# Optimization experiments

Measured on AMD Instinct MI355X. Metric: run time of the kernel, lower is better.

Reference implementation:

```python
import jax, jax.numpy as jnp
import numpy as np

B, T, D = 2, 2048, 2048
H, KVH, HD = 32, 8, 64
N_REP = H // KVH


def setup_inputs() -> dict:
    key = jax.random.key(0)
    ks = jax.random.split(key, 7)
    x = jax.random.normal(ks[0], (B, T, D), dtype=jnp.float32)
    # rope tables: [max_seq, head_dim//2]
    cos = jax.random.uniform(ks[1], (T, HD // 2), dtype=jnp.float32, minval=-1.0, maxval=1.0)
    sin = jax.random.uniform(ks[2], (T, HD // 2), dtype=jnp.float32, minval=-1.0, maxval=1.0)
    s = 0.02
    wq = jax.random.normal(ks[3], (D, H * HD), dtype=jnp.float32) * s
    wk = jax.random.normal(ks[4], (D, KVH * HD), dtype=jnp.float32) * s
    wv = jax.random.normal(ks[5], (D, KVH * HD), dtype=jnp.float32) * s
    wo = jax.random.normal(ks[6], (H * HD, D), dtype=jnp.float32) * s
    return {"x": x, "cos": cos, "sin": sin, "wq": wq, "wk": wk, "wv": wv, "wo": wo}


def _rotate(t):
    h = t.shape[-1] // 2
    return jnp.concatenate([-t[..., h:], t[..., :h]], axis=-1)


def reference(x, cos, sin, wq, wk, wv, wo):
    b, t, _ = x.shape
    # projections -> [B, heads, T, HD]
    q = (x @ wq).reshape(b, t, H, HD).transpose(0, 2, 1, 3)
    k = (x @ wk).reshape(b, t, KVH, HD).transpose(0, 2, 1, 3)
    v = (x @ wv).reshape(b, t, KVH, HD).transpose(0, 2, 1, 3)
    # rope: cos/sin tiled (concat) to full head_dim, broadcast over batch/head
    cos_f = jnp.tile(cos[:t], (1, 2))[None, None]  # [1,1,T,HD]
    sin_f = jnp.tile(sin[:t], (1, 2))[None, None]
    q = q * cos_f + _rotate(q) * sin_f
    k = k * cos_f + _rotate(k) * sin_f
    # GQA: repeat kv heads
    k = jnp.repeat(k, N_REP, axis=1)
    v = jnp.repeat(v, N_REP, axis=1)
    scale = 1.0 / np.sqrt(HD).astype(np.float32)
    scores = jnp.einsum('bhqd,bhkd->bhqk', q, k) * scale
    causal = jnp.tril(jnp.ones((t, t), dtype=bool))
    scores = jnp.where(causal, scores, jnp.float32(-1e30))
    attn = jax.nn.softmax(scores, axis=-1)
    out = jnp.einsum('bhqk,bhkd->bhqd', attn, v)
    out = out.transpose(0, 2, 1, 3).reshape(b, t, H * HD)
    return out @ wo
```

## Files before the change

kernel.cpp:

```cpp
#include <hip/hip_runtime.h>
#include <hip/hip_bf16.h>
#include <cstdint>

typedef unsigned short u16;
typedef unsigned int u32;
typedef __bf16 bf16x8 __attribute__((ext_vector_type(8)));
typedef float f32x4 __attribute__((ext_vector_type(4)));
typedef float f32x16 __attribute__((ext_vector_type(16)));

#define BATCH 2
#define SEQ 2048
#define DMODEL 2048
#define NH 32
#define NKVH 8
#define HD 64
#define NQROWS (BATCH*SEQ)
#define QCOLS (NH*HD)
#define KVCOLS (NKVH*HD)
#define NCAT (QCOLS+2*KVCOLS)

static __device__ __forceinline__ u16 f2bf(float f) {
  u32 u = __float_as_uint(f);
  return (u16)((u + 0x7fffu + ((u >> 16) & 1u)) >> 16);
}

#define GLOAD16(gp, lp) __builtin_amdgcn_global_load_lds( \
    (const __attribute__((address_space(1))) void*)(gp),  \
    (__attribute__((address_space(3))) void*)(lp), 16, 0, 0)

__global__ __launch_bounds__(256) void k_cvt_bf16(const float* __restrict__ in,
                                                  u16* __restrict__ out, int n4) {
  int i = blockIdx.x * 256 + threadIdx.x;
  if (i >= n4) return;
  float4 v = reinterpret_cast<const float4*>(in)[i];
  ushort4 o;
  o.x = f2bf(v.x); o.y = f2bf(v.y); o.z = f2bf(v.z); o.w = f2bf(v.w);
  reinterpret_cast<ushort4*>(out)[i] = o;
}

__global__ __launch_bounds__(256) void k_transpose_w(const float* __restrict__ in,
                                                     u16* __restrict__ out, int R, int C) {
  __shared__ float tile[32][33];
  int c0 = blockIdx.x * 32, r0 = blockIdx.y * 32;
  int tx = threadIdx.x, ty = threadIdx.y;
#pragma unroll
  for (int i = 0; i < 4; i++)
    tile[ty * 4 + i][tx] = in[(size_t)(r0 + ty * 4 + i) * C + c0 + tx];
  __syncthreads();
#pragma unroll
  for (int i = 0; i < 4; i++)
    out[(size_t)(c0 + ty * 4 + i) * R + r0 + tx] = f2bf(tile[tx][ty * 4 + i]);
}

template<int EPI>
__global__ __launch_bounds__(256) void k_gemm(const u16* __restrict__ A,
                                              const u16* __restrict__ BT,
                                              void* __restrict__ Cout,
                                              int M, int N, int K,
                                              const float* __restrict__ cosb,
                                              const float* __restrict__ sinb,
                                              u16* __restrict__ dstK,
                                              u16* __restrict__ dstV) {
  __shared__ __align__(16) u16 As[2][128 * 32];
  __shared__ __align__(16) u16 Bs[2][128 * 32];
  const int tid = threadIdx.x;
  const int w = tid >> 6, l = tid & 63;
  const int l15 = l & 15, l4 = l >> 4;

  const int nwg = gridDim.x * gridDim.y;
  int hwid = blockIdx.y * gridDim.x + blockIdx.x;
  int wk = (hwid & 7) * (nwg >> 3) + (hwid >> 3);
  const int bx = wk % gridDim.x, by = wk / gridDim.x;

  const int m0 = by * 128, n0 = bx * 128;
  const int wr = w >> 1, wc = w & 1;

  const u16* ga = A + (size_t)(m0 + w * 32 + (l >> 2)) * K + (l & 3) * 8;
  const u16* gb = BT + (size_t)(n0 + w * 32 + (l >> 2)) * K + (l & 3) * 8;
  const int af_off = (wr * 64 + l15) * 32 + l4 * 8;
  const int bf_off = (wc * 64 + l15) * 32 + l4 * 8;

  auto stage = [&](int buf, int kt) {
    const u16* ga_ = ga + kt;
    const u16* gb_ = gb + kt;
    u16* asb = &As[buf][w * 1024];
    u16* bsb = &Bs[buf][w * 1024];
    GLOAD16(ga_, asb);
    GLOAD16(ga_ + 16 * (size_t)K, asb + 512);
    GLOAD16(gb_, bsb);
    GLOAD16(gb_ + 16 * (size_t)K, bsb + 512);
  };

  f32x4 acc[4][4] = {};
  stage(0, 0);
  __syncthreads();

  int cur = 0;
  for (int kt = 0; kt < K; kt += 32) {
    if (kt + 32 < K) stage(cur ^ 1, kt + 32);
    bf16x8 af[4], bfv[4];
#pragma unroll
    for (int mi = 0; mi < 4; mi++)
      af[mi] = *reinterpret_cast<const bf16x8*>(&As[cur][af_off + mi * 512]);
#pragma unroll
    for (int ni = 0; ni < 4; ni++)
      bfv[ni] = *reinterpret_cast<const bf16x8*>(&Bs[cur][bf_off + ni * 512]);
#pragma unroll
    for (int mi = 0; mi < 4; mi++)
#pragma unroll
      for (int ni = 0; ni < 4; ni++)
        acc[mi][ni] = __builtin_amdgcn_mfma_f32_16x16x32_bf16(af[mi], bfv[ni], acc[mi][ni], 0, 0, 0);
    __syncthreads();
    cur ^= 1;
  }

  const int row0 = m0 + wr * 64 + l4 * 4;
  const int col0 = n0 + wc * 64 + l15;
  if constexpr (EPI == 1) {
    float* C = (float*)Cout;
#pragma unroll
    for (int mi = 0; mi < 4; mi++)
#pragma unroll
      for (int ni = 0; ni < 4; ni++)
#pragma unroll
        for (int j = 0; j < 4; j++)
          C[(size_t)(row0 + mi * 16 + j) * N + col0 + ni * 16] = acc[mi][ni][j];
  } else {
    if (n0 < QCOLS + KVCOLS) {
#pragma unroll
      for (int mi = 0; mi < 4; mi++)
#pragma unroll
        for (int j = 0; j < 4; j++) {
          int t = (row0 + mi * 16 + j) & (SEQ - 1);
#pragma unroll
          for (int ni = 0; ni < 2; ni++) {
            int d = ni * 16 + l15;
            float c = cosb[t * 32 + d], s = sinb[t * 32 + d];
            float a = acc[mi][ni][j], bb = acc[mi][ni + 2][j];
            acc[mi][ni][j]     = a * c - bb * s;
            acc[mi][ni + 2][j] = bb * c + a * s;
          }
        }
      if (n0 < QCOLS) {
        const float QSC = 0.125f * 1.44269504088896f;
        u16* C = (u16*)Cout;
#pragma unroll
        for (int mi = 0; mi < 4; mi++)
#pragma unroll
          for (int ni = 0; ni < 4; ni++)
#pragma unroll
            for (int j = 0; j < 4; j++)
              C[(size_t)(row0 + mi * 16 + j) * QCOLS + col0 + ni * 16] = f2bf(acc[mi][ni][j] * QSC);
      } else {
        int kc0 = col0 - QCOLS;
#pragma unroll
        for (int mi = 0; mi < 4; mi++)
#pragma unroll
          for (int ni = 0; ni < 4; ni++)
#pragma unroll
            for (int j = 0; j < 4; j++)
              dstK[(size_t)(row0 + mi * 16 + j) * KVCOLS + kc0 + ni * 16] = f2bf(acc[mi][ni][j]);
      }
    } else {
      int vc0 = col0 - (QCOLS + KVCOLS);
#pragma unroll
      for (int mi = 0; mi < 4; mi++) {
        int row = row0 + mi * 16;
        int b = row >> 11, t = row & (SEQ - 1);
#pragma unroll
        for (int ni = 0; ni < 4; ni++) {
          ushort4 v;
          v.x = f2bf(acc[mi][ni][0]);
          v.y = f2bf(acc[mi][ni][1]);
          v.z = f2bf(acc[mi][ni][2]);
          v.w = f2bf(acc[mi][ni][3]);
          *reinterpret_cast<ushort4*>(&dstV[((size_t)b * KVCOLS + vc0 + ni * 16) * SEQ + t]) = v;
        }
      }
    }
  }
}

__global__ __launch_bounds__(128, 3) void k_attn(const u16* __restrict__ Q,
                                                 const u16* __restrict__ K,
                                                 const u16* __restrict__ VT,
                                                 u16* __restrict__ AO) {
  __shared__ __align__(16) u16 Ks[2][4096];
  __shared__ __align__(16) u16 Vs[2][4096];
  const int tid = threadIdx.x;
  const int w = tid >> 6, l = tid & 63;
  const int lo = l & 31, hi = l >> 5;
  const int bh = blockIdx.y;
  const int b = bh >> 5, h = bh & 31, g = h >> 2;
  const int srow = l >> 3;
  const int scol = l & 7;

  const u16* Kbase = K + ((size_t)b * SEQ) * KVCOLS + g * 64;
  const u16* Vbase = VT + ((size_t)(b * KVCOLS + g * 64)) * SEQ;

  for (int half = 0; half < 2; half++) {
    const int qt = half ? (31 - blockIdx.x) : blockIdx.x;
    const int qbase = qt * 64 + w * 32;
    const int nkc = qt + 1;
    const int qloc = w * 32 + lo;

    bf16x8 qf[4];
    {
      const u16* qp = Q + (size_t)(b * SEQ + qbase + lo) * QCOLS + h * 64 + hi * 8;
#pragma unroll
      for (int kb = 0; kb < 4; kb++)
        qf[kb] = *reinterpret_cast<const bf16x8*>(qp + kb * 16);
    }
    f32x16 oacc[2] = {};
    float ls0 = 0.f, ls1 = 0.f;

#pragma unroll
    for (int i = 0; i < 4; i++) {
      int r = w * 32 + i * 8 + srow;
      int cs = scol ^ (srow & 7);
      GLOAD16(Kbase + (size_t)r * KVCOLS + cs * 8, &Ks[0][(w * 32 + i * 8) * 64 + l * 8]);
      GLOAD16(Vbase + (size_t)r * SEQ + cs * 8, &Vs[0][(w * 32 + i * 8) * 64 + l * 8]);
    }
    __syncthreads();

    for (int kc = 0; kc < nkc; kc++) {
      const int bi = kc & 1;
      if (kc + 1 < nkc) {
#pragma unroll
        for (int i = 0; i < 4; i++) {
          int r = w * 32 + i * 8 + srow;
          int cs = scol ^ (srow & 7);
          GLOAD16(Kbase + (size_t)((kc + 1) * 64 + r) * KVCOLS + cs * 8,
                  &Ks[bi ^ 1][(w * 32 + i * 8) * 64 + l * 8]);
          GLOAD16(Vbase + (size_t)r * SEQ + (kc + 1) * 64 + cs * 8,
                  &Vs[bi ^ 1][(w * 32 + i * 8) * 64 + l * 8]);
        }
      }
      f32x16 sacc[2] = {};
      __builtin_amdgcn_s_setprio(1);
#pragma unroll
      for (int t = 0; t < 2; t++) {
#pragma unroll
        for (int kb = 0; kb < 4; kb++) {
          int row = t * 32 + lo;
          int slot = (2 * kb + hi) ^ (lo & 7);
          bf16x8 kf = *reinterpret_cast<const bf16x8*>(&Ks[bi][row * 64 + slot * 8]);
          sacc[t] = __builtin_amdgcn_mfma_f32_32x32x16_bf16(kf, qf[kb], sacc[t], 0, 0, 0);
        }
      }
      __builtin_amdgcn_s_setprio(0);

      const bool diag = (kc == qt);
      u32 u[2][4][2];
#pragma unroll
      for (int t = 0; t < 2; t++) {
        float pv[16];
#pragma unroll
        for (int r = 0; r < 16; r++) {
          float e = exp2f(sacc[t][r]);
          if (diag) {
            int kvoff = t * 32 + (r & 3) + 8 * (r >> 2) + 4 * hi;
            if (kvoff > qloc) e = 0.f;
          }
          pv[r] = e;
          if (t == 0) ls0 += e; else ls1 += e;
        }
#pragma unroll
        for (int qd = 0; qd < 4; qd++)
#pragma unroll
          for (int hh = 0; hh < 2; hh++) {
            u32 uu;
            asm("v_cvt_pk_bf16_f32 %0, %1, %2"
                : "=v"(uu) : "v"(pv[qd * 4 + 2 * hh]), "v"(pv[qd * 4 + 2 * hh + 1]));
            u[t][qd][hh] = uu;
          }
      }

#pragma unroll
      for (int km = 0; km < 4; km++) {
        const int t = km >> 1, p = km & 1;
        u32 a0 = u[t][2 * p][0], b0 = u[t][2 * p + 1][0];
        u32 a1 = u[t][2 * p][1], b1 = u[t][2 * p + 1][1];
        asm("v_permlane32_swap_b32 %0, %1" : "+v"(a0), "+v"(b0));
        asm("v_permlane32_swap_b32 %0, %1" : "+v"(a1), "+v"(b1));
        union { u32 uu[4]; bf16x8 v; } pa;
        pa.uu[0] = a0; pa.uu[1] = a1; pa.uu[2] = b0; pa.uu[3] = b1;
        __builtin_amdgcn_s_setprio(1);
#pragma unroll
        for (int td = 0; td < 2; td++) {
          int row = td * 32 + lo;
          int slot = (2 * km + hi) ^ (lo & 7);
          bf16x8 vf = *reinterpret_cast<const bf16x8*>(&Vs[bi][row * 64 + slot * 8]);
          oacc[td] = __builtin_amdgcn_mfma_f32_32x32x16_bf16(pa.v, vf, oacc[td], 0, 0, 0);
        }
        __builtin_amdgcn_s_setprio(0);
      }
      __syncthreads();
    }
    float tot = ls0 + ls1;
    tot += __shfl_xor(tot, 32);
#pragma unroll
    for (int r = 0; r < 16; r++) {
      int qr = (r & 3) + 8 * (r >> 2) + 4 * hi;
      float den = __shfl(tot, qr);
      float rv = __builtin_amdgcn_rcpf(den);
      size_t rowbase = (size_t)(b * SEQ + qbase + qr) * QCOLS + h * 64 + lo;
      AO[rowbase]      = f2bf(oacc[0][r] * rv);
      AO[rowbase + 32] = f2bf(oacc[1][r] * rv);
    }
  }
}

extern "C" void kernel_launch(void* const* d_in, const int* in_sizes, int n_in,
                              void* d_out, int out_size, void* d_ws, size_t ws_size,
                              hipStream_t stream) {
  const float* x    = (const float*)d_in[0];
  const float* cosb = (const float*)d_in[1];
  const float* sinb = (const float*)d_in[2];
  const float* wq   = (const float*)d_in[3];
  const float* wk   = (const float*)d_in[4];
  const float* wv   = (const float*)d_in[5];
  const float* wo   = (const float*)d_in[6];
  float* out = (float*)d_out;

  char* ws = (char*)d_ws;
  size_t off = 0;
  auto alloc = [&](size_t bytes) -> void* {
    void* p = ws + off;
    off += (bytes + 255) & ~(size_t)255;
    return p;
  };
  u16* xb    = (u16*)alloc((size_t)NQROWS * DMODEL * 2);
  u16* wcatT = (u16*)alloc((size_t)NCAT * DMODEL * 2);
  u16* woT   = (u16*)alloc((size_t)DMODEL * QCOLS * 2);
  u16* Qb    = (u16*)alloc((size_t)NQROWS * QCOLS * 2);
  u16* Kb    = (u16*)alloc((size_t)NQROWS * KVCOLS * 2);
  u16* VTb   = (u16*)alloc((size_t)BATCH * KVCOLS * SEQ * 2);
  u16* AO    = (u16*)alloc((size_t)NQROWS * QCOLS * 2);

  k_cvt_bf16<<<dim3(NQROWS * DMODEL / 4 / 256), dim3(256), 0, stream>>>(x, xb, NQROWS * DMODEL / 4);
  k_transpose_w<<<dim3(QCOLS / 32, DMODEL / 32), dim3(32, 8), 0, stream>>>(wq, wcatT, DMODEL, QCOLS);
  k_transpose_w<<<dim3(KVCOLS / 32, DMODEL / 32), dim3(32, 8), 0, stream>>>(wk, wcatT + (size_t)QCOLS * DMODEL, DMODEL, KVCOLS);
  k_transpose_w<<<dim3(KVCOLS / 32, DMODEL / 32), dim3(32, 8), 0, stream>>>(wv, wcatT + (size_t)(QCOLS + KVCOLS) * DMODEL, DMODEL, KVCOLS);
  k_transpose_w<<<dim3(DMODEL / 32, QCOLS / 32), dim3(32, 8), 0, stream>>>(wo, woT, QCOLS, DMODEL);

  k_gemm<3><<<dim3(NCAT / 128, NQROWS / 128), 256, 0, stream>>>(
      xb, wcatT, Qb, NQROWS, NCAT, DMODEL, cosb, sinb, Kb, VTb);

  k_attn<<<dim3(16, BATCH * NH), 128, 0, stream>>>(Qb, Kb, VTb, AO);

  k_gemm<1><<<dim3(DMODEL / 128, NQROWS / 128), 256, 0, stream>>>(
      AO, woT, out, NQROWS, DMODEL, QCOLS, nullptr, nullptr, nullptr, nullptr);
}
```

Baseline: 210.4 us.

## Merge weight transposes into one launch and split attention into per-tile blocks

The four weight-transpose launches become one kernel that picks its source matrix from the block index. The attention kernel drops the paired-tile loop, where each block handled q-tile i and 31-i for causal balance. It now launches one block per q-tile, heaviest first, doubling the grid to 32x64 blocks. This removes launch overhead and raises parallelism, but gives up the explicit load balancing and relies on the scheduler to place the uneven work.

```diff
diff --git a/kernel.cpp b/kernel.cpp
--- a/kernel.cpp
+++ b/kernel.cpp
@@ -38,18 +38,40 @@
   reinterpret_cast<ushort4*>(out)[i] = o;
 }
 
-__global__ __launch_bounds__(256) void k_transpose_w(const float* __restrict__ in,
-                                                     u16* __restrict__ out, int R, int C) {
+__global__ __launch_bounds__(256) void k_transpose_all(const float* __restrict__ wq,
+                                                       const float* __restrict__ wk,
+                                                       const float* __restrict__ wv,
+                                                       const float* __restrict__ wo,
+                                                       u16* __restrict__ wcatT,
+                                                       u16* __restrict__ woT) {
   __shared__ float tile[32][33];
-  int c0 = blockIdx.x * 32, r0 = blockIdx.y * 32;
-  int tx = threadIdx.x, ty = threadIdx.y;
+  const int tidx = blockIdx.x;
+  const float* src; u16* dst; int C, c0, r0;
+  if (tidx < 4096) {
+    src = wq; dst = wcatT; C = QCOLS;
+    c0 = (tidx & 63) * 32; r0 = (tidx >> 6) * 32;
+  } else if (tidx < 5120) {
+    int t2 = tidx - 4096;
+    src = wk; dst = wcatT + (size_t)QCOLS * DMODEL; C = KVCOLS;
+    c0 = (t2 & 15) * 32; r0 = (t2 >> 4) * 32;
+  } else if (tidx < 6144) {
+    int t2 = tidx - 5120;
+    src = wv; dst = wcatT + (size_t)(QCOLS + KVCOLS) * DMODEL; C = KVCOLS;
+    c0 = (t2 & 15) * 32; r0 = (t2 >> 4) * 32;
+  } else {
+    int t2 = tidx - 6144;
+    src = wo; dst = woT; C = DMODEL;
+    c0 = (t2 & 63) * 32; r0 = (t2 >> 6) * 32;
+  }
+  const int R = 2048;
+  int tx = threadIdx.x & 31, ty = threadIdx.x >> 5;
 #pragma unroll
   for (int i = 0; i < 4; i++)
-    tile[ty * 4 + i][tx] = in[(size_t)(r0 + ty * 4 + i) * C + c0 + tx];
+    tile[ty * 4 + i][tx] = src[(size_t)(r0 + ty * 4 + i) * C + c0 + tx];
   __syncthreads();
 #pragma unroll
   for (int i = 0; i < 4; i++)
-    out[(size_t)(c0 + ty * 4 + i) * R + r0 + tx] = f2bf(tile[tx][ty * 4 + i]);
+    dst[(size_t)(c0 + ty * 4 + i) * R + r0 + tx] = f2bf(tile[tx][ty * 4 + i]);
 }
 
 template<int EPI>
@@ -198,116 +220,114 @@
   const u16* Kbase = K + ((size_t)b * SEQ) * KVCOLS + g * 64;
   const u16* Vbase = VT + ((size_t)(b * KVCOLS + g * 64)) * SEQ;
 
-  for (int half = 0; half < 2; half++) {
-    const int qt = half ? (31 - blockIdx.x) : blockIdx.x;
-    const int qbase = qt * 64 + w * 32;
-    const int nkc = qt + 1;
-    const int qloc = w * 32 + lo;
-
-    bf16x8 qf[4];
-    {
-      const u16* qp = Q + (size_t)(b * SEQ + qbase + lo) * QCOLS + h * 64 + hi * 8;
-#pragma unroll
-      for (int kb = 0; kb < 4; kb++)
-        qf[kb] = *reinterpret_cast<const bf16x8*>(qp + kb * 16);
-    }
-    f32x16 oacc[2] = {};
-    float ls0 = 0.f, ls1 = 0.f;
-
-#pragma unroll
-    for (int i = 0; i < 4; i++) {
-      int r = w * 32 + i * 8 + srow;
-      int cs = scol ^ (srow & 7);
-      GLOAD16(Kbase + (size_t)r * KVCOLS + cs * 8, &Ks[0][(w * 32 + i * 8) * 64 + l * 8]);
-      GLOAD16(Vbase + (size_t)r * SEQ + cs * 8, &Vs[0][(w * 32 + i * 8) * 64 + l * 8]);
+  const int qt = 31 - blockIdx.x;
+  const int qbase = qt * 64 + w * 32;
+  const int nkc = qt + 1;
+  const int qloc = w * 32 + lo;
+
+  bf16x8 qf[4];
+  {
+    const u16* qp = Q + (size_t)(b * SEQ + qbase + lo) * QCOLS + h * 64 + hi * 8;
+#pragma unroll
+    for (int kb = 0; kb < 4; kb++)
+      qf[kb] = *reinterpret_cast<const bf16x8*>(qp + kb * 16);
+  }
+  f32x16 oacc[2] = {};
+  float ls0 = 0.f, ls1 = 0.f;
+
+#pragma unroll
+  for (int i = 0; i < 4; i++) {
+    int r = w * 32 + i * 8 + srow;
+    int cs = scol ^ (srow & 7);
+    GLOAD16(Kbase + (size_t)r * KVCOLS + cs * 8, &Ks[0][(w * 32 + i * 8) * 64 + l * 8]);
+    GLOAD16(Vbase + (size_t)r * SEQ + cs * 8, &Vs[0][(w * 32 + i * 8) * 64 + l * 8]);
+  }
+  __syncthreads();
+
+  for (int kc = 0; kc < nkc; kc++) {
+    const int bi = kc & 1;
+    if (kc + 1 < nkc) {
+#pragma unroll
+      for (int i = 0; i < 4; i++) {
+        int r = w * 32 + i * 8 + srow;
+        int cs = scol ^ (srow & 7);
+        GLOAD16(Kbase + (size_t)((kc + 1) * 64 + r) * KVCOLS + cs * 8,
+                &Ks[bi ^ 1][(w * 32 + i * 8) * 64 + l * 8]);
+        GLOAD16(Vbase + (size_t)r * SEQ + (kc + 1) * 64 + cs * 8,
+                &Vs[bi ^ 1][(w * 32 + i * 8) * 64 + l * 8]);
+      }
+    }
+    f32x16 sacc[2] = {};
+    __builtin_amdgcn_s_setprio(1);
+#pragma unroll
+    for (int t = 0; t < 2; t++) {
+#pragma unroll
+      for (int kb = 0; kb < 4; kb++) {
+        int row = t * 32 + lo;
+        int slot = (2 * kb + hi) ^ (lo & 7);
+        bf16x8 kf = *reinterpret_cast<const bf16x8*>(&Ks[bi][row * 64 + slot * 8]);
+        sacc[t] = __builtin_amdgcn_mfma_f32_32x32x16_bf16(kf, qf[kb], sacc[t], 0, 0, 0);
+      }
+    }
+    __builtin_amdgcn_s_setprio(0);
+
+    const bool diag = (kc == qt);
+    u32 u[2][4][2];
+#pragma unroll
+    for (int t = 0; t < 2; t++) {
+      float pv[16];
+#pragma unroll
+      for (int r = 0; r < 16; r++) {
+        float e = exp2f(sacc[t][r]);
+        if (diag) {
+          int kvoff = t * 32 + (r & 3) + 8 * (r >> 2) + 4 * hi;
+          if (kvoff > qloc) e = 0.f;
+        }
+        pv[r] = e;
+        if (t == 0) ls0 += e; else ls1 += e;
+      }
+#pragma unroll
+      for (int qd = 0; qd < 4; qd++)
+#pragma unroll
+        for (int hh = 0; hh < 2; hh++) {
+          u32 uu;
+          asm("v_cvt_pk_bf16_f32 %0, %1, %2"
+              : "=v"(uu) : "v"(pv[qd * 4 + 2 * hh]), "v"(pv[qd * 4 + 2 * hh + 1]));
+          u[t][qd][hh] = uu;
+        }
+    }
+
+#pragma unroll
+    for (int km = 0; km < 4; km++) {
+      const int t = km >> 1, p = km & 1;
+      u32 a0 = u[t][2 * p][0], b0 = u[t][2 * p + 1][0];
+      u32 a1 = u[t][2 * p][1], b1 = u[t][2 * p + 1][1];
+      asm("v_permlane32_swap_b32 %0, %1" : "+v"(a0), "+v"(b0));
+      asm("v_permlane32_swap_b32 %0, %1" : "+v"(a1), "+v"(b1));
+      union { u32 uu[4]; bf16x8 v; } pa;
+      pa.uu[0] = a0; pa.uu[1] = a1; pa.uu[2] = b0; pa.uu[3] = b1;
+      __builtin_amdgcn_s_setprio(1);
+#pragma unroll
+      for (int td = 0; td < 2; td++) {
+        int row = td * 32 + lo;
+        int slot = (2 * km + hi) ^ (lo & 7);
+        bf16x8 vf = *reinterpret_cast<const bf16x8*>(&Vs[bi][row * 64 + slot * 8]);
+        oacc[td] = __builtin_amdgcn_mfma_f32_32x32x16_bf16(pa.v, vf, oacc[td], 0, 0, 0);
+      }
+      __builtin_amdgcn_s_setprio(0);
     }
     __syncthreads();
-
-    for (int kc = 0; kc < nkc; kc++) {
-      const int bi = kc & 1;
-      if (kc + 1 < nkc) {
-#pragma unroll
-        for (int i = 0; i < 4; i++) {
-          int r = w * 32 + i * 8 + srow;
-          int cs = scol ^ (srow & 7);
-          GLOAD16(Kbase + (size_t)((kc + 1) * 64 + r) * KVCOLS + cs * 8,
-                  &Ks[bi ^ 1][(w * 32 + i * 8) * 64 + l * 8]);
-          GLOAD16(Vbase + (size_t)r * SEQ + (kc + 1) * 64 + cs * 8,
-                  &Vs[bi ^ 1][(w * 32 + i * 8) * 64 + l * 8]);
-        }
-      }
-      f32x16 sacc[2] = {};
-      __builtin_amdgcn_s_setprio(1);
-#pragma unroll
-      for (int t = 0; t < 2; t++) {
-#pragma unroll
-        for (int kb = 0; kb < 4; kb++) {
-          int row = t * 32 + lo;
-          int slot = (2 * kb + hi) ^ (lo & 7);
-          bf16x8 kf = *reinterpret_cast<const bf16x8*>(&Ks[bi][row * 64 + slot * 8]);
-          sacc[t] = __builtin_amdgcn_mfma_f32_32x32x16_bf16(kf, qf[kb], sacc[t], 0, 0, 0);
-        }
-      }
-      __builtin_amdgcn_s_setprio(0);
-
-      const bool diag = (kc == qt);
-      u32 u[2][4][2];
-#pragma unroll
-      for (int t = 0; t < 2; t++) {
-        float pv[16];
-#pragma unroll
-        for (int r = 0; r < 16; r++) {
-          float e = exp2f(sacc[t][r]);
-          if (diag) {
-            int kvoff = t * 32 + (r & 3) + 8 * (r >> 2) + 4 * hi;
-            if (kvoff > qloc) e = 0.f;
-          }
-          pv[r] = e;
-          if (t == 0) ls0 += e; else ls1 += e;
-        }
-#pragma unroll
-        for (int qd = 0; qd < 4; qd++)
-#pragma unroll
-          for (int hh = 0; hh < 2; hh++) {
-            u32 uu;
-            asm("v_cvt_pk_bf16_f32 %0, %1, %2"
-                : "=v"(uu) : "v"(pv[qd * 4 + 2 * hh]), "v"(pv[qd * 4 + 2 * hh + 1]));
-            u[t][qd][hh] = uu;
-          }
-      }
-
-#pragma unroll
-      for (int km = 0; km < 4; km++) {
-        const int t = km >> 1, p = km & 1;
-        u32 a0 = u[t][2 * p][0], b0 = u[t][2 * p + 1][0];
-        u32 a1 = u[t][2 * p][1], b1 = u[t][2 * p + 1][1];
-        asm("v_permlane32_swap_b32 %0, %1" : "+v"(a0), "+v"(b0));
-        asm("v_permlane32_swap_b32 %0, %1" : "+v"(a1), "+v"(b1));
-        union { u32 uu[4]; bf16x8 v; } pa;
-        pa.uu[0] = a0; pa.uu[1] = a1; pa.uu[2] = b0; pa.uu[3] = b1;
-        __builtin_amdgcn_s_setprio(1);
-#pragma unroll
-        for (int td = 0; td < 2; td++) {
-          int row = td * 32 + lo;
-          int slot = (2 * km + hi) ^ (lo & 7);
-          bf16x8 vf = *reinterpret_cast<const bf16x8*>(&Vs[bi][row * 64 + slot * 8]);
-          oacc[td] = __builtin_amdgcn_mfma_f32_32x32x16_bf16(pa.v, vf, oacc[td], 0, 0, 0);
-        }
-        __builtin_amdgcn_s_setprio(0);
-      }
-      __syncthreads();
-    }
-    float tot = ls0 + ls1;
-    tot += __shfl_xor(tot, 32);
-#pragma unroll
-    for (int r = 0; r < 16; r++) {
-      int qr = (r & 3) + 8 * (r >> 2) + 4 * hi;
-      float den = __shfl(tot, qr);
-      float rv = __builtin_amdgcn_rcpf(den);
-      size_t rowbase = (size_t)(b * SEQ + qbase + qr) * QCOLS + h * 64 + lo;
-      AO[rowbase]      = f2bf(oacc[0][r] * rv);
-      AO[rowbase + 32] = f2bf(oacc[1][r] * rv);
-    }
+  }
+  float tot = ls0 + ls1;
+  tot += __shfl_xor(tot, 32);
+#pragma unroll
+  for (int r = 0; r < 16; r++) {
+    int qr = (r & 3) + 8 * (r >> 2) + 4 * hi;
+    float den = __shfl(tot, qr);
+    float rv = __builtin_amdgcn_rcpf(den);
+    size_t rowbase = (size_t)(b * SEQ + qbase + qr) * QCOLS + h * 64 + lo;
+    AO[rowbase]      = f2bf(oacc[0][r] * rv);
+    AO[rowbase + 32] = f2bf(oacc[1][r] * rv);
   }
 }
 
@@ -339,15 +359,12 @@
   u16* AO    = (u16*)alloc((size_t)NQROWS * QCOLS * 2);
 
   k_cvt_bf16<<<dim3(NQROWS * DMODEL / 4 / 256), dim3(256), 0, stream>>>(x, xb, NQROWS * DMODEL / 4);
-  k_transpose_w<<<dim3(QCOLS / 32, DMODEL / 32), dim3(32, 8), 0, stream>>>(wq, wcatT, DMODEL, QCOLS);
-  k_transpose_w<<<dim3(KVCOLS / 32, DMODEL / 32), dim3(32, 8), 0, stream>>>(wk, wcatT + (size_t)QCOLS * DMODEL, DMODEL, KVCOLS);
-  k_transpose_w<<<dim3(KVCOLS / 32, DMODEL / 32), dim3(32, 8), 0, stream>>>(wv, wcatT + (size_t)(QCOLS + KVCOLS) * DMODEL, DMODEL, KVCOLS);
-  k_transpose_w<<<dim3(DMODEL / 32, QCOLS / 32), dim3(32, 8), 0, stream>>>(wo, woT, QCOLS, DMODEL);
+  k_transpose_all<<<dim3(10240), dim3(256), 0, stream>>>(wq, wk, wv, wo, wcatT, woT);
 
   k_gemm<3><<<dim3(NCAT / 128, NQROWS / 128), 256, 0, stream>>>(
       xb, wcatT, Qb, NQROWS, NCAT, DMODEL, cosb, sinb, Kb, VTb);
 
-  k_attn<<<dim3(16, BATCH * NH), 128, 0, stream>>>(Qb, Kb, VTb, AO);
+  k_attn<<<dim3(32, BATCH * NH), 128, 0, stream>>>(Qb, Kb, VTb, AO);
 
   k_gemm<1><<<dim3(DMODEL / 128, NQROWS / 128), 256, 0, stream>>>(
       AO, woT, out, NQROWS, DMODEL, QCOLS, nullptr, nullptr, nullptr, nullptr);
```

Result: slower. 272.2 us (+29.4%).
